# Kernel tuning notes

Hardware: AMD Instinct MI355X
Metric: run time of the kernel (lower is better)

Reference implementation:

```python
import jax, jax.numpy as jnp
import numpy as np

N_NODES = 50000
N_EDGES = 800000
F_IN = 32
HID = 64
K = 4  # Chebyshev order in GConvLSTM(node_features, hidden, 4)


def setup_inputs() -> dict:
    key = jax.random.key(0)
    ks = jax.random.split(key, 14)
    x = jax.random.normal(ks[0], (N_NODES, F_IN), dtype=jnp.float32)
    edge_index = jax.random.randint(ks[1], (2, N_EDGES), 0, N_NODES, dtype=jnp.int64)
    edge_weight = jax.random.uniform(ks[2], (N_EDGES,), dtype=jnp.float32)
    s = 0.05
    # gate order: i, f, c, o
    Wx = jax.random.normal(ks[3], (4, K, F_IN, HID), dtype=jnp.float32) * s  # ChebConv weights on x
    bx = jax.random.normal(ks[4], (4, HID), dtype=jnp.float32) * s          # ChebConv biases on x
    Wh = jax.random.normal(ks[5], (4, K, HID, HID), dtype=jnp.float32) * s  # ChebConv weights on h
    bh = jax.random.normal(ks[6], (4, HID), dtype=jnp.float32) * s          # ChebConv biases on h
    wc = jax.random.normal(ks[7], (3, HID), dtype=jnp.float32) * s          # peephole w_c_i, w_c_f, w_c_o
    bg = jax.random.normal(ks[8], (4, HID), dtype=jnp.float32) * s          # gate biases b_i, b_f, b_c, b_o
    lin_w = jax.random.normal(ks[9], (HID, 1), dtype=jnp.float32) * s
    lin_b = jax.random.normal(ks[10], (1,), dtype=jnp.float32) * s
    return {"x": x, "edge_index": edge_index, "edge_weight": edge_weight,
            "Wx": Wx, "bx": bx, "Wh": Wh, "bh": bh, "wc": wc, "bg": bg,
            "lin_w": lin_w, "lin_b": lin_b}


def _cheb_norm(edge_index, edge_weight, num_nodes):
    # ChebConv.__norm__, sym normalization, lambda_max=2.0:
    # L_hat off-diagonal = -D^{-1/2} A D^{-1/2}, diagonal = 0.
    src, dst = edge_index[0], edge_index[1]
    deg = jax.ops.segment_sum(edge_weight, src, num_segments=num_nodes)
    d_inv_sqrt = jnp.where(deg > 0, jax.lax.rsqrt(jnp.maximum(deg, 1e-30)), 0.0)
    norm = -d_inv_sqrt[src] * edge_weight * d_inv_sqrt[dst]
    return src, dst, norm


def _cheb_conv(v, src, dst, norm, W, b, num_nodes):
    # ChebConv forward: out = sum_k T_k(L_hat) v @ W[k] + b, with propagate
    # = segment_sum of norm * v[src] at dst.
    def prop(t):
        return jax.ops.segment_sum(norm[:, None] * t[src], dst, num_segments=num_nodes)
    Tx0 = v
    out = Tx0 @ W[0]
    Tx1 = prop(Tx0)
    out = out + Tx1 @ W[1]
    for k in range(2, W.shape[0]):
        Tx2 = 2.0 * prop(Tx1) - Tx0
        out = out + Tx2 @ W[k]
        Tx0, Tx1 = Tx1, Tx2
    return out + b


def reference(x, edge_index, edge_weight, Wx, bx, Wh, bh, wc, bg, lin_w, lin_b):
    N = x.shape[0]
    src, dst, norm = _cheb_norm(edge_index, edge_weight, N)
    H = jnp.zeros((N, Wh.shape[-1]), dtype=x.dtype)
    C = jnp.zeros((N, Wh.shape[-1]), dtype=x.dtype)

    def gate(g, v_state):
        return (_cheb_conv(x, src, dst, norm, Wx[g], bx[g], N)
                + _cheb_conv(v_state, src, dst, norm, Wh[g], bh[g], N))

    I = jax.nn.sigmoid(gate(0, H) + wc[0] * C + bg[0])
    F = jax.nn.sigmoid(gate(1, H) + wc[1] * C + bg[1])
    T = jnp.tanh(gate(2, H) + bg[2])
    C = F * C + I * T
    O = jax.nn.sigmoid(gate(3, H) + wc[2] * C + bg[3])
    H = O * jnp.tanh(C)
    # dropout(p=0.25) is identity at inference; linear head HID -> 1
    return H @ lin_w + lin_b
```

## Files before the change

### kernel.cpp

```cpp
#include <hip/hip_runtime.h>
#include <math.h>


#define NT 256
#define NCH 64
#define RSH 20480
#define RSF 16384

typedef __attribute__((ext_vector_type(8))) short short8v;
typedef __attribute__((ext_vector_type(8))) unsigned short ushort8v;
typedef __attribute__((ext_vector_type(4))) float f32x4;

__device__ __forceinline__ short f2bf(float f) {
    unsigned u = __float_as_uint(f);
    u += 0x7FFFu + ((u >> 16) & 1u);
    return (short)(u >> 16);
}
__device__ __forceinline__ float bf2f(unsigned short b) {
    return __uint_as_float((unsigned)b << 16);
}

__global__ __launch_bounds__(1024)
void k_front(const int* __restrict__ src, const int* __restrict__ dst,
             const float* __restrict__ w, float* __restrict__ degPart,
             unsigned short* __restrict__ cntPart,
             const float* __restrict__ Wx, short* __restrict__ P,
             const float* __restrict__ x, short* __restrict__ xb,
             int nE, int N, int histB, int n4) {
    __shared__ float    s_deg[RSH];
    __shared__ unsigned s_cnt2[RSH / 2];
    const int bid = blockIdx.x;
    if (bid >= histB) {
        int idx = (bid - histB) * 1024 + (int)threadIdx.x;
        if (idx < 12 * 4 * 64) {
            int lane = idx & 63;
            int kt = (idx >> 6) & 3;
            int nt = idx >> 8;
            int gate = (nt < 4) ? 0 : (nt < 8) ? 2 : 3;
            int h = (nt & 3) * 16 + (lane & 15);
            int fb = (lane >> 4) * 8;
            short8v v;
#pragma unroll
            for (int j = 0; j < 8; ++j)
                v[j] = f2bf(Wx[((size_t)(gate * 4 + kt) * 32 + fb + j) * 64 + h]);
            *(reinterpret_cast<short8v*>(P) + idx) = v;
            return;
        }
        int i = idx - 12 * 4 * 64;
        if (i >= n4) return;
        const float4 v = *reinterpret_cast<const float4*>(x + (size_t)i * 4);
        short4 rb;
        rb.x = f2bf(v.x); rb.y = f2bf(v.y); rb.z = f2bf(v.z); rb.w = f2bf(v.w);
        *reinterpret_cast<short4*>(xb + (size_t)i * 4) = rb;
        return;
    }
    const int r = bid / NCH, b = bid % NCH;
    const int base = r * RSH;
    for (int i = threadIdx.x; i < RSH; i += 1024) s_deg[i] = 0.f;
    for (int i = threadIdx.x; i < RSH / 2; i += 1024) s_cnt2[i] = 0u;
    __syncthreads();
    const int chunk = (nE + NCH - 1) / NCH;
    const int e0 = b * chunk, e1 = min(e0 + chunk, nE);
    for (int e = e0 + (int)threadIdx.x; e < e1; e += 1024) {
        int s = src[e], d = dst[e];
        unsigned so = (unsigned)(s - base), dof = (unsigned)(d - base);
        if (so < RSH) atomicAdd(&s_deg[so], w[e]);
        if (dof < RSH) atomicAdd(&s_cnt2[dof >> 1], 1u << ((dof & 1) * 16));
    }
    __syncthreads();
    const int lim = min(RSH, N - base);
    for (int i = threadIdx.x; i < lim; i += 1024)
        degPart[(size_t)b * N + base + i] = s_deg[i];
    unsigned* cp32 = reinterpret_cast<unsigned*>(cntPart + (size_t)b * N + base);
    const int pairs = lim >> 1;
    for (int i = threadIdx.x; i < pairs; i += 1024) cp32[i] = s_cnt2[i];
    if ((lim & 1) && threadIdx.x == 0)
        cntPart[(size_t)b * N + base + lim - 1] =
            (unsigned short)(s_cnt2[lim >> 1] & 0xFFFFu);
}

__global__ __launch_bounds__(NT)
void k_reduce_scanA(const float* __restrict__ degPart,
                    const unsigned short* __restrict__ cntPart,
                    float* __restrict__ dinv, int* __restrict__ cnt,
                    int* __restrict__ rowptr, int* __restrict__ partials, int N) {
    __shared__ int s[NT];
    const int t = threadIdx.x;
    const int n0 = blockIdx.x * (NT * 2) + t * 2;
    float d0 = 0.f, d1 = 0.f;
    int c0 = 0, c1 = 0;
    if (n0 < N) {
#pragma unroll 8
        for (int b = 0; b < NCH; ++b) {
            const float2 dv = *reinterpret_cast<const float2*>(degPart + (size_t)b * N + n0);
            d0 += dv.x; d1 += dv.y;
            unsigned cc = *reinterpret_cast<const unsigned*>(cntPart + (size_t)b * N + n0);
            c0 += (int)(cc & 0xFFFFu); c1 += (int)(cc >> 16);
        }
        dinv[n0] = d0 > 0.f ? rsqrtf(d0) : 0.f;
        cnt[n0] = c0;
        if (n0 + 1 < N) {
            dinv[n0 + 1] = d1 > 0.f ? rsqrtf(d1) : 0.f;
            cnt[n0 + 1] = c1;
        } else c1 = 0;
    }
    int cs = c0 + c1;
    s[t] = cs;
    __syncthreads();
    for (int off = 1; off < NT; off <<= 1) {
        int u = (t >= off) ? s[t - off] : 0;
        __syncthreads();
        s[t] += u;
        __syncthreads();
    }
    int ex = s[t] - cs;
    if (n0 < N) {
        rowptr[n0] = ex;
        if (n0 + 1 < N) rowptr[n0 + 1] = ex + c0;
    }
    if (t == NT - 1) partials[blockIdx.x] = s[t];
}

__global__ __launch_bounds__(NT)
void k_scan_off(int* __restrict__ rowptr, const int* __restrict__ partials, int nb2,
                const unsigned short* __restrict__ cntPart, int* __restrict__ offs,
                int N) {
    __shared__ int sp[NT];
    const int t = threadIdx.x;
    int v = (t < (int)blockIdx.x && t < nb2) ? partials[t] : 0;
    sp[t] = v;
    __syncthreads();
    for (int off = NT / 2; off > 0; off >>= 1) {
        if (t < off) sp[t] += sp[t + off];
        __syncthreads();
    }
    const int prefix = sp[0];
    const int n0 = blockIdx.x * (NT * 2) + t * 2;
    if (n0 >= N) return;
    const bool has1 = (n0 + 1) < N;
    int s0 = rowptr[n0] + prefix;
    int s1 = has1 ? rowptr[n0 + 1] + prefix : 0;
    rowptr[n0] = s0;
    if (has1) rowptr[n0 + 1] = s1;
#pragma unroll 8
    for (int b = 0; b < NCH; ++b) {
        unsigned cc = *reinterpret_cast<const unsigned*>(cntPart + (size_t)b * N + n0);
        if (has1) {
            *reinterpret_cast<int2*>(offs + (size_t)b * N + n0) = make_int2(s0, s1);
        } else {
            offs[(size_t)b * N + n0] = s0;
        }
        s0 += (int)(cc & 0xFFFFu);
        s1 += (int)(cc >> 16);
    }
}

__global__ __launch_bounds__(1024)
void k_fill2(const int* __restrict__ src, const int* __restrict__ dst,
             const float* __restrict__ w, const float* __restrict__ dinv,
             const int* __restrict__ offs, int2* __restrict__ entries,
             int nE, int N) {
    __shared__ int s_cur[RSF];
    const int r = blockIdx.x / NCH, b = blockIdx.x % NCH;
    const int base = r * RSF;
    const int lim = min(RSF, N - base);
    for (int i = threadIdx.x; i < lim; i += 1024)
        s_cur[i] = offs[(size_t)b * N + base + i];
    __syncthreads();
    const int chunk = (nE + NCH - 1) / NCH;
    const int e0 = b * chunk, e1 = min(e0 + chunk, nE);
    for (int e = e0 + (int)threadIdx.x; e < e1; e += 1024) {
        int d = dst[e];
        unsigned dof = (unsigned)(d - base);
        if (dof < RSF) {
            int s = src[e];
            float nv = -dinv[s] * w[e] * dinv[d];
            int pos = atomicAdd(&s_cur[dof], 1);
            entries[pos] = make_int2(s, __float_as_int(nv));
        }
    }
}

__device__ __forceinline__ void bf8_fma(float* acc, ushort8v v, float s) {
#pragma unroll
    for (int j = 0; j < 8; ++j)
        acc[j] = fmaf(s, bf2f(v[j]), acc[j]);
}

__global__ __launch_bounds__(256)
void k_gather_bf(const unsigned short* __restrict__ tb,
                 const unsigned short* __restrict__ subb,
                 short* __restrict__ outb,
                 const int* __restrict__ rowptr, const int* __restrict__ cnt,
                 const int2* __restrict__ entries, float scale, int N) {
    int idx = blockIdx.x * blockDim.x + threadIdx.x;
    if (idx >= N * 8) return;
    int n = idx >> 3, tq = idx & 3, half = (idx >> 2) & 1;
    int beg = rowptr[n], end = beg + cnt[n];
    float acc0[8] = {0, 0, 0, 0, 0, 0, 0, 0};
    float acc1[8] = {0, 0, 0, 0, 0, 0, 0, 0};
    int i = beg + half;
    for (; i + 6 < end; i += 8) {
        int2 e0 = entries[i];
        int2 e1 = entries[i + 2];
        int2 e2 = entries[i + 4];
        int2 e3 = entries[i + 6];
        ushort8v v0 = *reinterpret_cast<const ushort8v*>(tb + (size_t)e0.x * 32 + tq * 8);
        ushort8v v1 = *reinterpret_cast<const ushort8v*>(tb + (size_t)e1.x * 32 + tq * 8);
        ushort8v v2 = *reinterpret_cast<const ushort8v*>(tb + (size_t)e2.x * 32 + tq * 8);
        ushort8v v3 = *reinterpret_cast<const ushort8v*>(tb + (size_t)e3.x * 32 + tq * 8);
        bf8_fma(acc0, v0, __int_as_float(e0.y));
        bf8_fma(acc1, v1, __int_as_float(e1.y));
        bf8_fma(acc0, v2, __int_as_float(e2.y));
        bf8_fma(acc1, v3, __int_as_float(e3.y));
    }
    for (; i < end; i += 2) {
        int2 e0 = entries[i];
        ushort8v v0 = *reinterpret_cast<const ushort8v*>(tb + (size_t)e0.x * 32 + tq * 8);
        bf8_fma(acc0, v0, __int_as_float(e0.y));
    }
    float r[8];
#pragma unroll
    for (int j = 0; j < 8; ++j) {
        r[j] = acc0[j] + acc1[j];
        r[j] += __shfl_xor(r[j], 4);
    }
    if (!half) {
        if (subb) {
            ushort8v sv = *reinterpret_cast<const ushort8v*>(subb + (size_t)n * 32 + tq * 8);
#pragma unroll
            for (int j = 0; j < 8; ++j) r[j] = fmaf(scale, r[j], -bf2f(sv[j]));
        } else {
#pragma unroll
            for (int j = 0; j < 8; ++j) r[j] *= scale;
        }
        short8v rb;
#pragma unroll
        for (int j = 0; j < 8; ++j) rb[j] = f2bf(r[j]);
        *reinterpret_cast<short8v*>(outb + (size_t)n * 32 + tq * 8) = rb;
    }
}

__device__ __forceinline__ float sigf(float x) {
    return __builtin_amdgcn_rcpf(1.f + __builtin_amdgcn_exp2f(-1.4426950408889634f * x));
}
__device__ __forceinline__ float tanhf_fast(float x) {
    float e = __builtin_amdgcn_exp2f(2.8853900817779268f * x);
    return 1.f - 2.f * __builtin_amdgcn_rcpf(e + 1.f);
}

__global__ __launch_bounds__(256)
void k_final_g3(const short* __restrict__ xb, const short* __restrict__ t1b,
                const unsigned short* __restrict__ t2b,
                const short* __restrict__ P,
                const int* __restrict__ rowptr, const int* __restrict__ cnt,
                const int2* __restrict__ entries,
                const float* __restrict__ bx, const float* __restrict__ bh,
                const float* __restrict__ wc, const float* __restrict__ bg,
                const float* __restrict__ lin_w, const float* __restrict__ lin_b,
                float* __restrict__ out, int N) {
    const int wave = threadIdx.x >> 6, lane = threadIdx.x & 63;
    const int nb = blockIdx.x * 64 + wave * 16;
    const int rc = min(nb + (lane & 15), N - 1);
    const int ko = (lane >> 4) * 8;

    int beg = rowptr[rc], end = beg + cnt[rc];
    float acc0[8] = {0, 0, 0, 0, 0, 0, 0, 0};
    float acc1[8] = {0, 0, 0, 0, 0, 0, 0, 0};
    int i = beg;
    for (; i + 3 < end; i += 4) {
        int2 e0 = entries[i];
        int2 e1 = entries[i + 1];
        int2 e2 = entries[i + 2];
        int2 e3 = entries[i + 3];
        ushort8v v0 = *reinterpret_cast<const ushort8v*>(t2b + (size_t)e0.x * 32 + ko);
        ushort8v v1 = *reinterpret_cast<const ushort8v*>(t2b + (size_t)e1.x * 32 + ko);
        ushort8v v2 = *reinterpret_cast<const ushort8v*>(t2b + (size_t)e2.x * 32 + ko);
        ushort8v v3 = *reinterpret_cast<const ushort8v*>(t2b + (size_t)e3.x * 32 + ko);
        bf8_fma(acc0, v0, __int_as_float(e0.y));
        bf8_fma(acc1, v1, __int_as_float(e1.y));
        bf8_fma(acc0, v2, __int_as_float(e2.y));
        bf8_fma(acc1, v3, __int_as_float(e3.y));
    }
    for (; i < end; ++i) {
        int2 e0 = entries[i];
        ushort8v v0 = *reinterpret_cast<const ushort8v*>(t2b + (size_t)e0.x * 32 + ko);
        bf8_fma(acc0, v0, __int_as_float(e0.y));
    }

    short8v A0 = *reinterpret_cast<const short8v*>(xb  + (size_t)rc * 32 + ko);
    short8v A1 = *reinterpret_cast<const short8v*>(t1b + (size_t)rc * 32 + ko);
    short8v A2 = *reinterpret_cast<const short8v*>(
        reinterpret_cast<const short*>(t2b) + (size_t)rc * 32 + ko);
    short8v A3;
#pragma unroll
    for (int j = 0; j < 8; ++j)
        A3[j] = f2bf(2.f * (acc0[j] + acc1[j]) - bf2f((unsigned short)A1[j]));

    const short8v* Pv = reinterpret_cast<const short8v*>(P);
    f32x4 acc[12];
#pragma unroll
    for (int nt = 0; nt < 12; ++nt) {
        const short8v* Pb = Pv + (size_t)nt * 4 * 64 + lane;
        f32x4 a = {0.f, 0.f, 0.f, 0.f};
        a = __builtin_amdgcn_mfma_f32_16x16x32_bf16(A0, Pb[0],   a, 0, 0, 0);
        a = __builtin_amdgcn_mfma_f32_16x16x32_bf16(A1, Pb[64],  a, 0, 0, 0);
        a = __builtin_amdgcn_mfma_f32_16x16x32_bf16(A2, Pb[128], a, 0, 0, 0);
        a = __builtin_amdgcn_mfma_f32_16x16x32_bf16(A3, Pb[192], a, 0, 0, 0);
        acc[nt] = a;
    }

    const int hq = lane & 15;
    const int ng = lane >> 4;
    const float lb = lin_b[0];
    float p[4] = {0.f, 0.f, 0.f, 0.f};
#pragma unroll
    for (int ht = 0; ht < 4; ++ht) {
        int h = ht * 16 + hq;
        float bI = bx[h] + bh[h] + bg[h];
        float bC = bx[128 + h] + bh[128 + h] + bg[128 + h];
        float bO = bx[192 + h] + bh[192 + h] + bg[192 + h];
        float w2 = wc[128 + h];
        float lw = lin_w[h];
#pragma unroll
        for (int r = 0; r < 4; ++r) {
            float I = sigf(acc[ht][r] + bI);
            float T = tanhf_fast(acc[4 + ht][r] + bC);
            float C = I * T;
            float O = sigf(acc[8 + ht][r] + bO + w2 * C);
            float H = O * tanhf_fast(C);
            p[r] = fmaf(H, lw, p[r]);
        }
    }
#pragma unroll
    for (int r = 0; r < 4; ++r) {
        float v = p[r];
        v += __shfl_xor(v, 1);
        v += __shfl_xor(v, 2);
        v += __shfl_xor(v, 4);
        v += __shfl_xor(v, 8);
        if (hq == 0) {
            int n = nb + ng * 4 + r;
            if (n < N) out[n] = v + lb;
        }
    }
}

extern "C" void kernel_launch(void* const* d_in, const int* in_sizes, int n_in,
                              void* d_out, int out_size, void* d_ws, size_t ws_size,
                              hipStream_t stream) {
    const float* x   = (const float*)d_in[0];
    const int*   ei  = (const int*)d_in[1];
    const float* ew  = (const float*)d_in[2];
    const float* Wx  = (const float*)d_in[3];
    const float* bx  = (const float*)d_in[4];
    const float* bh  = (const float*)d_in[6];
    const float* wcp = (const float*)d_in[7];
    const float* bg  = (const float*)d_in[8];
    const float* lw  = (const float*)d_in[9];
    const float* lb  = (const float*)d_in[10];
    float* out = (float*)d_out;

    const int N  = in_sizes[0] / 32;
    const int nE = in_sizes[2];
    const int* src = ei;
    const int* dst = ei + nE;

    char* ws = (char*)d_ws;
    size_t off = 0;
    float* dinv    = (float*)(ws + off); off += (size_t)N * 4;
    int*   cnt     = (int*)(ws + off);   off += (size_t)N * 4;
    int*   rowptr  = (int*)(ws + off);   off += (size_t)N * 4;
    int*   partials= (int*)(ws + off);   off += 1024 * 4;
    short* P       = (short*)(ws + off); off += 12 * 4 * 64 * 8 * 2;
    int2*  entries = (int2*)(ws + off);  off += (size_t)nE * 8;
    float* degPart = (float*)(ws + off); off += (size_t)NCH * N * 4;
    unsigned short* cntPart = (unsigned short*)(ws + off); off += (size_t)NCH * N * 2;
    short* xbuf    = (short*)(ws + off); off += (size_t)N * 32 * 2;
    short* Tx1b    = (short*)(ws + off); off += (size_t)N * 32 * 2;
    short* Tx2b    = (short*)(ws + off); off += (size_t)N * 32 * 2;

    int* offs = (int*)degPart;

    const int nRangeH = (N + RSH - 1) / RSH;
    const int nRangeF = (N + RSF - 1) / RSF;
    const int histB = nRangeH * NCH;
    const int n4 = N * 8;
    const int xbB = (12 * 4 * 64 + n4 + 1023) / 1024;
    const int nb2 = (N + NT * 2 - 1) / (NT * 2);

    k_front<<<histB + xbB, 1024, 0, stream>>>(src, dst, ew, degPart, cntPart,
                                              Wx, P, x, xbuf, nE, N, histB, n4);
    k_reduce_scanA<<<nb2, NT, 0, stream>>>(degPart, cntPart, dinv, cnt, rowptr,
                                           partials, N);
    k_scan_off<<<nb2, NT, 0, stream>>>(rowptr, partials, nb2, cntPart, offs, N);
    k_fill2<<<nRangeF * NCH, 1024, 0, stream>>>(src, dst, ew, dinv, offs,
                                                entries, nE, N);

    const int gb = (N * 8 + NT - 1) / NT;
    k_gather_bf<<<gb, NT, 0, stream>>>((const unsigned short*)xbuf, nullptr,
                                       Tx1b, rowptr, cnt, entries, 1.f, N);
    k_gather_bf<<<gb, NT, 0, stream>>>((const unsigned short*)Tx1b,
                                       (const unsigned short*)xbuf,
                                       Tx2b, rowptr, cnt, entries, 2.f, N);

    const int fb = (N + 63) / 64;
    k_final_g3<<<fb, NT, 0, stream>>>(xbuf, Tx1b, (const unsigned short*)Tx2b, P,
                                      rowptr, cnt, entries, bx, bh, wcp, bg,
                                      lw, lb, out, N);
}
```

Before: 103.4 us.

## Merge scan kernels with grid barrier and widen gather edge parallelism

Fuses the two prefix-scan kernels into one, using an atomic flag spin barrier to exchange block partials and caching the count histogram in shared memory instead of re-reading it. The gather kernel now uses 16 threads per node, splitting edges four ways to expose more memory parallelism. The fill range size is enlarged to cut the number of ranges. This risks deadlock if not all blocks are co-resident, adds a memset launch, and adds shuffle reductions.

```diff
diff --git a/kernel.cpp b/kernel.cpp
--- a/kernel.cpp
+++ b/kernel.cpp
@@ -5,7 +5,7 @@
 #define NT 256
 #define NCH 64
 #define RSH 20480
-#define RSF 16384
+#define RSF 20480
 
 typedef __attribute__((ext_vector_type(8))) short short8v;
 typedef __attribute__((ext_vector_type(8))) unsigned short ushort8v;
@@ -80,11 +80,13 @@
 }
 
 __global__ __launch_bounds__(NT)
-void k_reduce_scanA(const float* __restrict__ degPart,
-                    const unsigned short* __restrict__ cntPart,
-                    float* __restrict__ dinv, int* __restrict__ cnt,
-                    int* __restrict__ rowptr, int* __restrict__ partials, int N) {
-    __shared__ int s[NT];
+void k_scan_merged(const float* __restrict__ degPart,
+                   const unsigned short* __restrict__ cntPart,
+                   float* __restrict__ dinv, int* __restrict__ cnt,
+                   int* __restrict__ rowptr, int* __restrict__ partials,
+                   int* __restrict__ flag, int* __restrict__ offs, int N) {
+    __shared__ unsigned s_c[NCH * NT];
+    __shared__ int sp[NT];
     const int t = threadIdx.x;
     const int n0 = blockIdx.x * (NT * 2) + t * 2;
     float d0 = 0.f, d1 = 0.f;
@@ -95,6 +97,7 @@
             const float2 dv = *reinterpret_cast<const float2*>(degPart + (size_t)b * N + n0);
             d0 += dv.x; d1 += dv.y;
             unsigned cc = *reinterpret_cast<const unsigned*>(cntPart + (size_t)b * N + n0);
+            s_c[b * NT + t] = cc;
             c0 += (int)(cc & 0xFFFFu); c1 += (int)(cc >> 16);
         }
         dinv[n0] = d0 > 0.f ? rsqrtf(d0) : 0.f;
@@ -105,29 +108,30 @@
         } else c1 = 0;
     }
     int cs = c0 + c1;
-    s[t] = cs;
+    sp[t] = cs;
     __syncthreads();
     for (int off = 1; off < NT; off <<= 1) {
-        int u = (t >= off) ? s[t - off] : 0;
+        int u = (t >= off) ? sp[t - off] : 0;
         __syncthreads();
-        s[t] += u;
+        sp[t] += u;
         __syncthreads();
     }
-    int ex = s[t] - cs;
-    if (n0 < N) {
-        rowptr[n0] = ex;
-        if (n0 + 1 < N) rowptr[n0 + 1] = ex + c0;
-    }
-    if (t == NT - 1) partials[blockIdx.x] = s[t];
-}
-
-__global__ __launch_bounds__(NT)
-void k_scan_off(int* __restrict__ rowptr, const int* __restrict__ partials, int nb2,
-                const unsigned short* __restrict__ cntPart, int* __restrict__ offs,
-                int N) {
-    __shared__ int sp[NT];
-    const int t = threadIdx.x;
-    int v = (t < (int)blockIdx.x && t < nb2) ? partials[t] : 0;
+    const int ex = sp[t] - cs;
+    const int total = sp[NT - 1];
+    __syncthreads();
+    if (t == 0) {
+        __hip_atomic_store(&partials[blockIdx.x], total, __ATOMIC_RELEASE,
+                           __HIP_MEMORY_SCOPE_AGENT);
+        atomicAdd(flag, 1);
+        while (__hip_atomic_load(flag, __ATOMIC_ACQUIRE,
+                                 __HIP_MEMORY_SCOPE_AGENT) < (int)gridDim.x)
+            __builtin_amdgcn_s_sleep(1);
+    }
+    __syncthreads();
+    int v = (t < (int)blockIdx.x)
+                ? __hip_atomic_load(&partials[t], __ATOMIC_ACQUIRE,
+                                    __HIP_MEMORY_SCOPE_AGENT)
+                : 0;
     sp[t] = v;
     __syncthreads();
     for (int off = NT / 2; off > 0; off >>= 1) {
@@ -135,16 +139,15 @@
         __syncthreads();
     }
     const int prefix = sp[0];
-    const int n0 = blockIdx.x * (NT * 2) + t * 2;
     if (n0 >= N) return;
     const bool has1 = (n0 + 1) < N;
-    int s0 = rowptr[n0] + prefix;
-    int s1 = has1 ? rowptr[n0 + 1] + prefix : 0;
+    int s0 = ex + prefix;
+    int s1 = has1 ? ex + c0 + prefix : 0;
     rowptr[n0] = s0;
     if (has1) rowptr[n0 + 1] = s1;
 #pragma unroll 8
     for (int b = 0; b < NCH; ++b) {
-        unsigned cc = *reinterpret_cast<const unsigned*>(cntPart + (size_t)b * N + n0);
+        unsigned cc = s_c[b * NT + t];
         if (has1) {
             *reinterpret_cast<int2*>(offs + (size_t)b * N + n0) = make_int2(s0, s1);
         } else {
@@ -194,17 +197,17 @@
                  const int* __restrict__ rowptr, const int* __restrict__ cnt,
                  const int2* __restrict__ entries, float scale, int N) {
     int idx = blockIdx.x * blockDim.x + threadIdx.x;
-    if (idx >= N * 8) return;
-    int n = idx >> 3, tq = idx & 3, half = (idx >> 2) & 1;
+    if (idx >= N * 16) return;
+    int n = idx >> 4, tq = idx & 3, qr = (idx >> 2) & 3;
     int beg = rowptr[n], end = beg + cnt[n];
     float acc0[8] = {0, 0, 0, 0, 0, 0, 0, 0};
     float acc1[8] = {0, 0, 0, 0, 0, 0, 0, 0};
-    int i = beg + half;
-    for (; i + 6 < end; i += 8) {
+    int i = beg + qr;
+    for (; i + 12 < end; i += 16) {
         int2 e0 = entries[i];
-        int2 e1 = entries[i + 2];
-        int2 e2 = entries[i + 4];
-        int2 e3 = entries[i + 6];
+        int2 e1 = entries[i + 4];
+        int2 e2 = entries[i + 8];
+        int2 e3 = entries[i + 12];
         ushort8v v0 = *reinterpret_cast<const ushort8v*>(tb + (size_t)e0.x * 32 + tq * 8);
         ushort8v v1 = *reinterpret_cast<const ushort8v*>(tb + (size_t)e1.x * 32 + tq * 8);
         ushort8v v2 = *reinterpret_cast<const ushort8v*>(tb + (size_t)e2.x * 32 + tq * 8);
@@ -214,7 +217,7 @@
         bf8_fma(acc0, v2, __int_as_float(e2.y));
         bf8_fma(acc1, v3, __int_as_float(e3.y));
     }
-    for (; i < end; i += 2) {
+    for (; i < end; i += 4) {
         int2 e0 = entries[i];
         ushort8v v0 = *reinterpret_cast<const ushort8v*>(tb + (size_t)e0.x * 32 + tq * 8);
         bf8_fma(acc0, v0, __int_as_float(e0.y));
@@ -224,8 +227,9 @@
     for (int j = 0; j < 8; ++j) {
         r[j] = acc0[j] + acc1[j];
         r[j] += __shfl_xor(r[j], 4);
-    }
-    if (!half) {
+        r[j] += __shfl_xor(r[j], 8);
+    }
+    if (qr == 0) {
         if (subb) {
             ushort8v sv = *reinterpret_cast<const ushort8v*>(subb + (size_t)n * 32 + tq * 8);
 #pragma unroll
@@ -372,6 +376,7 @@
     int*   cnt     = (int*)(ws + off);   off += (size_t)N * 4;
     int*   rowptr  = (int*)(ws + off);   off += (size_t)N * 4;
     int*   partials= (int*)(ws + off);   off += 1024 * 4;
+    int*   flag    = (int*)(ws + off);   off += 256;
     short* P       = (short*)(ws + off); off += 12 * 4 * 64 * 8 * 2;
     int2*  entries = (int2*)(ws + off);  off += (size_t)nE * 8;
     float* degPart = (float*)(ws + off); off += (size_t)NCH * N * 4;
@@ -389,15 +394,15 @@
     const int xbB = (12 * 4 * 64 + n4 + 1023) / 1024;
     const int nb2 = (N + NT * 2 - 1) / (NT * 2);
 
+    hipMemsetAsync(flag, 0, 4, stream);
     k_front<<<histB + xbB, 1024, 0, stream>>>(src, dst, ew, degPart, cntPart,
                                               Wx, P, x, xbuf, nE, N, histB, n4);
-    k_reduce_scanA<<<nb2, NT, 0, stream>>>(degPart, cntPart, dinv, cnt, rowptr,
-                                           partials, N);
-    k_scan_off<<<nb2, NT, 0, stream>>>(rowptr, partials, nb2, cntPart, offs, N);
+    k_scan_merged<<<nb2, NT, 0, stream>>>(degPart, cntPart, dinv, cnt, rowptr,
+                                          partials, flag, offs, N);
     k_fill2<<<nRangeF * NCH, 1024, 0, stream>>>(src, dst, ew, dinv, offs,
                                                 entries, nE, N);
 
-    const int gb = (N * 8 + NT - 1) / NT;
+    const int gb = (N * 16 + NT - 1) / NT;
     k_gather_bf<<<gb, NT, 0, stream>>>((const unsigned short*)xbuf, nullptr,
                                        Tx1b, rowptr, cnt, entries, 1.f, N);
     k_gather_bf<<<gb, NT, 0, stream>>>((const unsigned short*)Tx1b,
```

Result: no change. 103.2 us (-0.2%).
